# Performance work log

Measured on AMD Instinct MI355X. Metric: run time of the kernel, lower is better.

Reference implementation:

```python
import jax, jax.numpy as jnp
import numpy as np

N_NODES = 50000
N_EDGES = 800000
IN_FEATS = 128
H_FEATS = 128
NUM_CLASSES = 16


def setup_inputs() -> dict:
    key = jax.random.key(0)
    ks = jax.random.split(key, 10)
    in_feat = jax.random.normal(ks[0], (N_NODES, IN_FEATS), dtype=jnp.float32)
    src = jax.random.randint(ks[1], (N_EDGES,), 0, N_NODES, dtype=jnp.int64)
    dst = jax.random.randint(ks[2], (N_EDGES,), 0, N_NODES, dtype=jnp.int64)
    def glorot(k, shape):
        lim = np.sqrt(6.0 / (shape[0] + shape[1]))
        return jax.random.uniform(k, shape, jnp.float32, -lim, lim)
    W_self1 = glorot(ks[3], (IN_FEATS, H_FEATS))
    W_neigh1 = glorot(ks[4], (IN_FEATS, H_FEATS))
    b1 = jnp.zeros((H_FEATS,), jnp.float32)
    W_self2 = glorot(ks[5], (H_FEATS, NUM_CLASSES))
    W_neigh2 = glorot(ks[6], (H_FEATS, NUM_CLASSES))
    b2 = jnp.zeros((NUM_CLASSES,), jnp.float32)
    return {"in_feat": in_feat, "src": src, "dst": dst,
            "W_self1": W_self1, "W_neigh1": W_neigh1, "b1": b1,
            "W_self2": W_self2, "W_neigh2": W_neigh2, "b2": b2}


def _mean_agg(h, src, dst, n_nodes):
    # sum of source features at each destination node, divided by in-degree
    summed = jax.ops.segment_sum(h[src], dst, num_segments=n_nodes)  # [N, d]
    deg = jax.ops.segment_sum(jnp.ones_like(dst, dtype=h.dtype), dst,
                              num_segments=n_nodes)                   # [N]
    return summed / jnp.maximum(deg, 1.0)[:, None]


def _sage_conv(h, src, dst, W_self, W_neigh, b):
    h_neigh = _mean_agg(h, src, dst, h.shape[0])
    return h @ W_self + h_neigh @ W_neigh + b


def reference(in_feat, src, dst, W_self1, W_neigh1, b1, W_self2, W_neigh2, b2):
    h = _sage_conv(in_feat, src, dst, W_self1, W_neigh1, b1)
    h = jax.nn.relu(h)
    h = _sage_conv(h, src, dst, W_self2, W_neigh2, b2)
    return h
```

## Files before the change

kernel.cpp:

```cpp
#include <hip/hip_runtime.h>

#define NF 128
#define BSH 8
#define CHUNK 4096

typedef __attribute__((ext_vector_type(8))) short short8;
typedef __attribute__((ext_vector_type(4))) float floatx4;

__device__ __forceinline__ unsigned short f2bf(float f) {
    unsigned u = __float_as_uint(f);
    u += 0x7fff + ((u >> 16) & 1);
    return (unsigned short)(u >> 16);
}
__device__ __forceinline__ unsigned pk2(float a, float b) {
    return (unsigned)f2bf(a) | ((unsigned)f2bf(b) << 16);
}
__device__ __forceinline__ float bflo(unsigned u) { return __uint_as_float(u << 16); }
__device__ __forceinline__ float bfhi(unsigned u) { return __uint_as_float(u & 0xffff0000u); }

__device__ __forceinline__ unsigned enc8(float f) {
    unsigned b = __float_as_uint(f);
    unsigned s = (b >> 24) & 0x80u;
    b &= 0x7fffffffu;
    unsigned t = b + 0x7FFFFu + ((b >> 20) & 1u);
    unsigned m = (t >= 0x3C800000u) ? (((t - 0x3C000000u) >> 20) & 0x7Fu) : 0u;
    return s | m;
}
__device__ __forceinline__ void dec4(float* acc, unsigned w) {
#pragma unroll
    for (int j = 0; j < 4; ++j) {
        unsigned u = (w >> (8 * j)) & 0xffu;
        acc[j] += __uint_as_float(((u & 0x80u) << 24) | ((u & 0x7fu) << 20));
    }
}


__global__ __launch_bounds__(256) void k_prep(const float* __restrict__ in_feat,
                                              const int* __restrict__ dst,
                                              const float* __restrict__ Ws1,
                                              const float* __restrict__ Wn1,
                                              const float* __restrict__ Ws2,
                                              const float* __restrict__ Wn2,
                                              unsigned short* __restrict__ featbf,
                                              unsigned char* __restrict__ feat8,
                                              unsigned short* __restrict__ W1t,
                                              unsigned short* __restrict__ W2t,
                                              int* __restrict__ cnt2,
                                              int nb_cvt, int nb_w, int E) {
    int b = blockIdx.x, tid = threadIdx.x;
    if (b < nb_cvt) {
        int i = b * 256 + tid;
        const float4* p = (const float4*)in_feat + (size_t)i * 2;
        float4 a = p[0], c = p[1];
        uint4 o;
        o.x = pk2(a.x, a.y); o.y = pk2(a.z, a.w);
        o.z = pk2(c.x, c.y); o.w = pk2(c.z, c.w);
        ((uint4*)featbf)[i] = o;
        uint2 q;
        q.x = enc8(a.x) | (enc8(a.y) << 8) | (enc8(a.z) << 16) | (enc8(a.w) << 24);
        q.y = enc8(c.x) | (enc8(c.y) << 8) | (enc8(c.z) << 16) | (enc8(c.w) << 24);
        ((uint2*)feat8)[i] = q;
    } else if (b < nb_cvt + nb_w) {
        int idx = (b - nb_cvt) * 256 + tid;
        if (idx < 128 * 256) {
            int n = idx >> 8, kk = idx & 255;
            float v = (kk < 128) ? Ws1[(size_t)kk * 128 + n]
                                 : Wn1[(size_t)(kk - 128) * 128 + n];
            W1t[idx] = f2bf(v);
        } else {
            int idx2 = idx - 128 * 256;
            if (idx2 < 32 * 128) {
                int n = idx2 >> 7, k = idx2 & 127;
                float v = (n < 16) ? Ws2[(size_t)k * 16 + n]
                                   : Wn2[(size_t)k * 16 + (n - 16)];
                W2t[idx2] = f2bf(v);
            }
        }
    } else {
        __shared__ int h[256];
        int c = b - nb_cvt - nb_w;
        h[tid] = 0;
        __syncthreads();
        int base = c * CHUNK;
        int n = min(CHUNK, E - base);
        for (int i = tid; i < n; i += 256) atomicAdd(&h[dst[base + i] >> BSH], 1);
        __syncthreads();
        cnt2[c * 256 + tid] = h[tid];
    }
}


__global__ __launch_bounds__(256) void k_cscan(const int* __restrict__ cnt2,
                                               int* __restrict__ goff,
                                               int* __restrict__ basep, int nc) {
    __shared__ int sw[4];
    int tid = threadIdx.x, lane = tid & 63, w = tid >> 6;
    int tot = 0;
    int c = 0;
    for (; c + 7 < nc; c += 8) {
        int v0 = cnt2[(c + 0) * 256 + tid], v1 = cnt2[(c + 1) * 256 + tid];
        int v2 = cnt2[(c + 2) * 256 + tid], v3 = cnt2[(c + 3) * 256 + tid];
        int v4 = cnt2[(c + 4) * 256 + tid], v5 = cnt2[(c + 5) * 256 + tid];
        int v6 = cnt2[(c + 6) * 256 + tid], v7 = cnt2[(c + 7) * 256 + tid];
        tot += ((v0 + v1) + (v2 + v3)) + ((v4 + v5) + (v6 + v7));
    }
    for (; c < nc; ++c) tot += cnt2[c * 256 + tid];

    int inc = tot;
#pragma unroll
    for (int d = 1; d < 64; d <<= 1) {
        int t = __shfl_up(inc, (unsigned)d, 64);
        if (lane >= d) inc += t;
    }
    if (lane == 63) sw[w] = inc;
    __syncthreads();
    int add = 0;
    for (int i = 0; i < w; ++i) add += sw[i];
    int ex = add + inc - tot;
    goff[tid] = ex;
    if (tid == 255) goff[256] = ex + tot;

    int run = ex;
    for (c = 0; c < nc; c += 8) {
        int v[8];
#pragma unroll
        for (int j = 0; j < 8; ++j)
            v[j] = (c + j < nc) ? cnt2[(c + j) * 256 + tid] : 0;
#pragma unroll
        for (int j = 0; j < 8; ++j) {
            if (c + j < nc) basep[(c + j) * 256 + tid] = run;
            run += v[j];
        }
    }
}


__global__ __launch_bounds__(256) void k_part(const int* __restrict__ src,
                                              const int* __restrict__ dst,
                                              const int* __restrict__ basep,
                                              unsigned* __restrict__ ebuf, int E) {
    __shared__ int cur[256];
    int tid = threadIdx.x;
    cur[tid] = basep[blockIdx.x * 256 + tid];
    __syncthreads();
    int base = blockIdx.x * CHUNK;
    int n = min(CHUNK, E - base);
    for (int i = tid; i < n; i += 256) {
        int dd = dst[base + i];
        int p = atomicAdd(&cur[dd >> BSH], 1);
        ebuf[p] = ((unsigned)(dd & 255) << 16) | (unsigned)src[base + i];
    }
}


__global__ __launch_bounds__(256) void k_fine(const unsigned* __restrict__ ebuf,
                                              const int* __restrict__ goff,
                                              int* __restrict__ off,
                                              int* __restrict__ csr, int N) {
    __shared__ int degL[256];
    __shared__ int offL[256];
    __shared__ int sw[4];
    int b = blockIdx.x, tid = threadIdx.x;
    int node0 = b << BSH;
    int e0 = goff[b], e1 = goff[b + 1];
    degL[tid] = 0;
    __syncthreads();
    for (int e = e0 + tid; e < e1; e += 256) atomicAdd(&degL[ebuf[e] >> 16], 1);
    __syncthreads();
    int lane = tid & 63, w = tid >> 6;
    int v = degL[tid], inc = v;
#pragma unroll
    for (int d = 1; d < 64; d <<= 1) {
        int t = __shfl_up(inc, (unsigned)d, 64);
        if (lane >= d) inc += t;
    }
    if (lane == 63) sw[w] = inc;
    __syncthreads();
    int add = 0;
    for (int i = 0; i < w; ++i) add += sw[i];
    int ex = add + inc - v;
    offL[tid] = ex;
    int idx = node0 + tid;
    if (idx <= N) off[idx] = e0 + ex;
    degL[tid] = 0;
    __syncthreads();
    for (int e = e0 + tid; e < e1; e += 256) {
        unsigned u = ebuf[e];
        int d = u >> 16;
        int pos = e0 + offL[d] + atomicAdd(&degL[d], 1);
        csr[pos] = (int)(u & 0xffffu);
    }
}


__global__ __launch_bounds__(256, 6) void k_agg1(const unsigned char* __restrict__ feat8,
                                                 const int* __restrict__ off,
                                                 const int* __restrict__ csr,
                                                 unsigned short* __restrict__ outm, int N) {
    int idx = blockIdx.x * 256 + threadIdx.x;
    int g = idx >> 4;
    int lane = idx & 15;
    if (g >= N) return;
    int s0 = off[g], s1 = off[g + 1];
    float acc[8];
#pragma unroll
    for (int i = 0; i < 8; ++i) acc[i] = 0.f;
    const uint2* F = (const uint2*)feat8;
    int e = s0;
    for (; e + 7 < s1; e += 8) {
        uint2 v0 = F[(size_t)csr[e + 0] * 16 + lane];
        uint2 v1 = F[(size_t)csr[e + 1] * 16 + lane];
        uint2 v2 = F[(size_t)csr[e + 2] * 16 + lane];
        uint2 v3 = F[(size_t)csr[e + 3] * 16 + lane];
        uint2 v4 = F[(size_t)csr[e + 4] * 16 + lane];
        uint2 v5 = F[(size_t)csr[e + 5] * 16 + lane];
        uint2 v6 = F[(size_t)csr[e + 6] * 16 + lane];
        uint2 v7 = F[(size_t)csr[e + 7] * 16 + lane];
        dec4(acc + 0, v0.x); dec4(acc + 4, v0.y);
        dec4(acc + 0, v1.x); dec4(acc + 4, v1.y);
        dec4(acc + 0, v2.x); dec4(acc + 4, v2.y);
        dec4(acc + 0, v3.x); dec4(acc + 4, v3.y);
        dec4(acc + 0, v4.x); dec4(acc + 4, v4.y);
        dec4(acc + 0, v5.x); dec4(acc + 4, v5.y);
        dec4(acc + 0, v6.x); dec4(acc + 4, v6.y);
        dec4(acc + 0, v7.x); dec4(acc + 4, v7.y);
    }
    if (e + 3 < s1) {
        uint2 v0 = F[(size_t)csr[e + 0] * 16 + lane];
        uint2 v1 = F[(size_t)csr[e + 1] * 16 + lane];
        uint2 v2 = F[(size_t)csr[e + 2] * 16 + lane];
        uint2 v3 = F[(size_t)csr[e + 3] * 16 + lane];
        dec4(acc + 0, v0.x); dec4(acc + 4, v0.y);
        dec4(acc + 0, v1.x); dec4(acc + 4, v1.y);
        dec4(acc + 0, v2.x); dec4(acc + 4, v2.y);
        dec4(acc + 0, v3.x); dec4(acc + 4, v3.y);
        e += 4;
    }
    for (; e < s1; ++e) {
        uint2 v = F[(size_t)csr[e] * 16 + lane];
        dec4(acc + 0, v.x); dec4(acc + 4, v.y);
    }
    float inv = __uint_as_float(0x7B800000u) / fmaxf((float)(s1 - s0), 1.0f);
    uint2 o;
    o.x = pk2(acc[0] * inv, acc[1] * inv);
    o.y = pk2(acc[2] * inv, acc[3] * inv);
    uint2 o2;
    o2.x = pk2(acc[4] * inv, acc[5] * inv);
    o2.y = pk2(acc[6] * inv, acc[7] * inv);
    uint2* op = (uint2*)(outm + (size_t)g * NF + lane * 8);
    op[0] = o;
    op[1] = o2;
}


__global__ __launch_bounds__(256) void k_gemm(const unsigned short* __restrict__ Abf,
                                              const unsigned short* __restrict__ Hbf,
                                              const unsigned short* __restrict__ W1t,
                                              const float* __restrict__ b1,
                                              const unsigned short* __restrict__ W2t,
                                              const float* __restrict__ b2,
                                              float* __restrict__ t2s,
                                              unsigned short* __restrict__ t2n, int M) {
    __shared__ float hL[64 * 140];
    int tid = threadIdx.x;
    int w = tid >> 6, lane = tid & 63;
    int q = lane >> 4, r = lane & 15;
    int row = blockIdx.x * 64 + w * 16 + r;
    int rowc = min(row, M - 1);

    floatx4 acc[8];
#pragma unroll
    for (int t = 0; t < 8; ++t) acc[t] = (floatx4){0.f, 0.f, 0.f, 0.f};

    const unsigned short* arow = Abf + (size_t)rowc * 128;
    const unsigned short* hrow = Hbf + (size_t)rowc * 128;

#pragma unroll
    for (int kc = 0; kc < 8; ++kc) {
        const unsigned short* ap = (kc < 4) ? (arow + kc * 32 + q * 8)
                                            : (hrow + (kc - 4) * 32 + q * 8);
        short8 a = *(const short8*)ap;
        const unsigned short* wp = W1t + kc * 32 + q * 8 + (size_t)r * 256;
#pragma unroll
        for (int t = 0; t < 8; ++t) {
            short8 b = *(const short8*)(wp + (size_t)t * 16 * 256);
            acc[t] = __builtin_amdgcn_mfma_f32_16x16x32_bf16(a, b, acc[t], 0, 0, 0);
        }
    }

#pragma unroll
    for (int i = 0; i < 4; ++i) {
        int lr = w * 16 + q * 4 + i;
#pragma unroll
        for (int t = 0; t < 8; ++t)
            hL[lr * 140 + t * 16 + r] = fmaxf(acc[t][i] + b1[t * 16 + r], 0.0f);
    }

    floatx4 acc2[2];
#pragma unroll
    for (int t = 0; t < 2; ++t) acc2[t] = (floatx4){0.f, 0.f, 0.f, 0.f};

#pragma unroll
    for (int kc = 0; kc < 4; ++kc) {
        const float* pa = hL + (w * 16 + r) * 140 + kc * 32 + q * 8;
        float4 fa = *(const float4*)pa;
        float4 fb = *(const float4*)(pa + 4);
        union { short8 s; uint4 u; } cv;
        cv.u = make_uint4(pk2(fa.x, fa.y), pk2(fa.z, fa.w),
                          pk2(fb.x, fb.y), pk2(fb.z, fb.w));
        const unsigned short* wp = W2t + kc * 32 + q * 8 + (size_t)r * 128;
#pragma unroll
        for (int t = 0; t < 2; ++t) {
            short8 b = *(const short8*)(wp + (size_t)t * 16 * 128);
            acc2[t] = __builtin_amdgcn_mfma_f32_16x16x32_bf16(cv.s, b, acc2[t], 0, 0, 0);
        }
    }

    int orow0 = blockIdx.x * 64 + w * 16 + q * 4;
    float bb = b2[r];
#pragma unroll
    for (int i = 0; i < 4; ++i) {
        int orow = orow0 + i;
        if (orow < M) {
            t2s[(size_t)orow * 16 + r] = acc2[0][i] + bb;
            t2n[(size_t)orow * 16 + r] = f2bf(acc2[1][i]);
        }
    }
}


__global__ __launch_bounds__(256, 6) void k_out(const float* __restrict__ t2s,
                                                const unsigned short* __restrict__ t2n,
                                                const int* __restrict__ off,
                                                const int* __restrict__ csr,
                                                float* __restrict__ out, int N) {
    int idx = blockIdx.x * 256 + threadIdx.x;
    int node = idx >> 2;
    if (node >= N) return;
    int ln = idx & 3;
    int s0 = off[node], s1 = off[node + 1];
    float acc[4];
#pragma unroll
    for (int i = 0; i < 4; ++i) acc[i] = 0.f;
    const uint2* T = (const uint2*)t2n;
    int e = s0;
    for (; e + 7 < s1; e += 8) {
        uint2 v0 = T[(size_t)csr[e + 0] * 4 + ln];
        uint2 v1 = T[(size_t)csr[e + 1] * 4 + ln];
        uint2 v2 = T[(size_t)csr[e + 2] * 4 + ln];
        uint2 v3 = T[(size_t)csr[e + 3] * 4 + ln];
        uint2 v4 = T[(size_t)csr[e + 4] * 4 + ln];
        uint2 v5 = T[(size_t)csr[e + 5] * 4 + ln];
        uint2 v6 = T[(size_t)csr[e + 6] * 4 + ln];
        uint2 v7 = T[(size_t)csr[e + 7] * 4 + ln];
        acc[0] += bflo(v0.x) + bflo(v1.x) + bflo(v2.x) + bflo(v3.x)
                + bflo(v4.x) + bflo(v5.x) + bflo(v6.x) + bflo(v7.x);
        acc[1] += bfhi(v0.x) + bfhi(v1.x) + bfhi(v2.x) + bfhi(v3.x)
                + bfhi(v4.x) + bfhi(v5.x) + bfhi(v6.x) + bfhi(v7.x);
        acc[2] += bflo(v0.y) + bflo(v1.y) + bflo(v2.y) + bflo(v3.y)
                + bflo(v4.y) + bflo(v5.y) + bflo(v6.y) + bflo(v7.y);
        acc[3] += bfhi(v0.y) + bfhi(v1.y) + bfhi(v2.y) + bfhi(v3.y)
                + bfhi(v4.y) + bfhi(v5.y) + bfhi(v6.y) + bfhi(v7.y);
    }
    for (; e < s1; ++e) {
        uint2 v = T[(size_t)csr[e] * 4 + ln];
        acc[0] += bflo(v.x); acc[1] += bfhi(v.x);
        acc[2] += bflo(v.y); acc[3] += bfhi(v.y);
    }
    float inv = 1.0f / fmaxf((float)(s1 - s0), 1.0f);
    const float4* sp = (const float4*)(t2s + (size_t)node * 16 + ln * 4);
    float4 sv = sp[0];
    float4 r;
    r.x = sv.x + acc[0] * inv;
    r.y = sv.y + acc[1] * inv;
    r.z = sv.z + acc[2] * inv;
    r.w = sv.w + acc[3] * inv;
    *(float4*)(out + (size_t)node * 16 + ln * 4) = r;
}


extern "C" void kernel_launch(void* const* d_in, const int* in_sizes, int n_in,
                              void* d_out, int out_size, void* d_ws, size_t ws_size,
                              hipStream_t stream) {
    const float* in_feat = (const float*)d_in[0];
    const int*   src     = (const int*)d_in[1];
    const int*   dst     = (const int*)d_in[2];
    const float* Ws1     = (const float*)d_in[3];
    const float* Wn1     = (const float*)d_in[4];
    const float* b1      = (const float*)d_in[5];
    const float* Ws2     = (const float*)d_in[6];
    const float* Wn2     = (const float*)d_in[7];
    const float* b2      = (const float*)d_in[8];
    float* outp = (float*)d_out;

    int N = in_sizes[0] / NF;
    int E = in_sizes[1];
    int nb = (N + 255) >> BSH;
    int nc = (E + CHUNK - 1) / CHUNK;

    char* ws = (char*)d_ws;
    size_t o = 0;
    auto alloc = [&](size_t bytes) -> char* {
        char* p = ws + o;
        o = (o + bytes + 255) & ~(size_t)255;
        return p;
    };
    int*      cnt2  = (int*)alloc((size_t)nc * 256 * 4);
    int*      basep = (int*)alloc((size_t)nc * 256 * 4);
    int*      goff  = (int*)alloc(257 * 4);
    int*      off   = (int*)alloc((size_t)(N + 1) * 4);
    int*      csr   = (int*)alloc((size_t)E * 4);
    unsigned* ebuf  = (unsigned*)alloc((size_t)E * 4);
    unsigned short* featbf = (unsigned short*)alloc((size_t)N * NF * 2);
    unsigned char*  feat8  = (unsigned char*)alloc((size_t)N * NF);
    unsigned short* hn1    = (unsigned short*)alloc((size_t)N * NF * 2);
    unsigned short* W1t    = (unsigned short*)alloc((size_t)128 * 256 * 2);
    unsigned short* W2t    = (unsigned short*)alloc((size_t)32 * 128 * 2);
    float*          t2s    = (float*)alloc((size_t)N * 16 * 4);
    unsigned short* t2n    = (unsigned short*)alloc((size_t)N * 16 * 2);

    int nb_cvt = (N * NF / 8 + 255) / 256;
    int nb_w = (128 * 256 + 32 * 128 + 255) / 256;
    k_prep<<<nb_cvt + nb_w + nc, 256, 0, stream>>>(in_feat, dst, Ws1, Wn1, Ws2, Wn2,
                                                   featbf, feat8, W1t, W2t, cnt2,
                                                   nb_cvt, nb_w, E);
    k_cscan<<<1, 256, 0, stream>>>(cnt2, goff, basep, nc);
    k_part<<<nc, 256, 0, stream>>>(src, dst, basep, ebuf, E);
    k_fine<<<nb, 256, 0, stream>>>(ebuf, goff, off, csr, N);

    k_agg1<<<(N * 16 + 255) / 256, 256, 0, stream>>>(feat8, off, csr, hn1, N);

    int gb_m = (N + 63) / 64;
    k_gemm<<<gb_m, 256, 0, stream>>>(featbf, hn1, W1t, b1, W2t, b2, t2s, t2n, N);
    k_out<<<(N * 4 + 255) / 256, 256, 0, stream>>>(t2s, t2n, off, csr, outp, N);
}
```

Baseline: 218.6 us.

## Split layer-1 aggregation into two feature-half passes for cache locality

The first aggregation kernel now launches two sets of blocks, one per 64-byte half of each node's fp8 feature row, with 8 lanes per node instead of 16. Each pass only gathers half of each 128-byte row, which roughly halves the gathered working set per pass and is meant to improve L2 hit rates on the random neighbor gathers. Outputs become single 16-byte stores. The trade-off is that the CSR offsets and indices are read twice. The output kernel's launch-bounds occupancy hint is also raised from 6 to 8.

```diff
diff --git a/kernel.cpp b/kernel.cpp
--- a/kernel.cpp
+++ b/kernel.cpp
@@ -196,26 +196,29 @@
 __global__ __launch_bounds__(256, 6) void k_agg1(const unsigned char* __restrict__ feat8,
                                                  const int* __restrict__ off,
                                                  const int* __restrict__ csr,
-                                                 unsigned short* __restrict__ outm, int N) {
-    int idx = blockIdx.x * 256 + threadIdx.x;
-    int g = idx >> 4;
-    int lane = idx & 15;
+                                                 unsigned short* __restrict__ hn1,
+                                                 int N, int pb) {
+    int b = blockIdx.x;
+    int half = (b >= pb) ? 1 : 0;
+    int idx = (b - half * pb) * 256 + threadIdx.x;
+    int g = idx >> 3;
+    int lane = idx & 7;
     if (g >= N) return;
     int s0 = off[g], s1 = off[g + 1];
+    const unsigned char* base = feat8 + half * 64 + lane * 8;
     float acc[8];
 #pragma unroll
     for (int i = 0; i < 8; ++i) acc[i] = 0.f;
-    const uint2* F = (const uint2*)feat8;
     int e = s0;
     for (; e + 7 < s1; e += 8) {
-        uint2 v0 = F[(size_t)csr[e + 0] * 16 + lane];
-        uint2 v1 = F[(size_t)csr[e + 1] * 16 + lane];
-        uint2 v2 = F[(size_t)csr[e + 2] * 16 + lane];
-        uint2 v3 = F[(size_t)csr[e + 3] * 16 + lane];
-        uint2 v4 = F[(size_t)csr[e + 4] * 16 + lane];
-        uint2 v5 = F[(size_t)csr[e + 5] * 16 + lane];
-        uint2 v6 = F[(size_t)csr[e + 6] * 16 + lane];
-        uint2 v7 = F[(size_t)csr[e + 7] * 16 + lane];
+        uint2 v0 = *(const uint2*)(base + (size_t)csr[e + 0] * 128);
+        uint2 v1 = *(const uint2*)(base + (size_t)csr[e + 1] * 128);
+        uint2 v2 = *(const uint2*)(base + (size_t)csr[e + 2] * 128);
+        uint2 v3 = *(const uint2*)(base + (size_t)csr[e + 3] * 128);
+        uint2 v4 = *(const uint2*)(base + (size_t)csr[e + 4] * 128);
+        uint2 v5 = *(const uint2*)(base + (size_t)csr[e + 5] * 128);
+        uint2 v6 = *(const uint2*)(base + (size_t)csr[e + 6] * 128);
+        uint2 v7 = *(const uint2*)(base + (size_t)csr[e + 7] * 128);
         dec4(acc + 0, v0.x); dec4(acc + 4, v0.y);
         dec4(acc + 0, v1.x); dec4(acc + 4, v1.y);
         dec4(acc + 0, v2.x); dec4(acc + 4, v2.y);
@@ -226,10 +229,10 @@
         dec4(acc + 0, v7.x); dec4(acc + 4, v7.y);
     }
     if (e + 3 < s1) {
-        uint2 v0 = F[(size_t)csr[e + 0] * 16 + lane];
-        uint2 v1 = F[(size_t)csr[e + 1] * 16 + lane];
-        uint2 v2 = F[(size_t)csr[e + 2] * 16 + lane];
-        uint2 v3 = F[(size_t)csr[e + 3] * 16 + lane];
+        uint2 v0 = *(const uint2*)(base + (size_t)csr[e + 0] * 128);
+        uint2 v1 = *(const uint2*)(base + (size_t)csr[e + 1] * 128);
+        uint2 v2 = *(const uint2*)(base + (size_t)csr[e + 2] * 128);
+        uint2 v3 = *(const uint2*)(base + (size_t)csr[e + 3] * 128);
         dec4(acc + 0, v0.x); dec4(acc + 4, v0.y);
         dec4(acc + 0, v1.x); dec4(acc + 4, v1.y);
         dec4(acc + 0, v2.x); dec4(acc + 4, v2.y);
@@ -237,19 +240,16 @@
         e += 4;
     }
     for (; e < s1; ++e) {
-        uint2 v = F[(size_t)csr[e] * 16 + lane];
+        uint2 v = *(const uint2*)(base + (size_t)csr[e] * 128);
         dec4(acc + 0, v.x); dec4(acc + 4, v.y);
     }
     float inv = __uint_as_float(0x7B800000u) / fmaxf((float)(s1 - s0), 1.0f);
-    uint2 o;
+    uint4 o;
     o.x = pk2(acc[0] * inv, acc[1] * inv);
     o.y = pk2(acc[2] * inv, acc[3] * inv);
-    uint2 o2;
-    o2.x = pk2(acc[4] * inv, acc[5] * inv);
-    o2.y = pk2(acc[6] * inv, acc[7] * inv);
-    uint2* op = (uint2*)(outm + (size_t)g * NF + lane * 8);
-    op[0] = o;
-    op[1] = o2;
+    o.z = pk2(acc[4] * inv, acc[5] * inv);
+    o.w = pk2(acc[6] * inv, acc[7] * inv);
+    *(uint4*)(hn1 + (size_t)g * NF + half * 64 + lane * 8) = o;
 }
 
 
@@ -329,7 +329,7 @@
 }
 
 
-__global__ __launch_bounds__(256, 6) void k_out(const float* __restrict__ t2s,
+__global__ __launch_bounds__(256, 8) void k_out(const float* __restrict__ t2s,
                                                 const unsigned short* __restrict__ t2n,
                                                 const int* __restrict__ off,
                                                 const int* __restrict__ csr,
@@ -428,7 +428,8 @@
     k_part<<<nc, 256, 0, stream>>>(src, dst, basep, ebuf, E);
     k_fine<<<nb, 256, 0, stream>>>(ebuf, goff, off, csr, N);
 
-    k_agg1<<<(N * 16 + 255) / 256, 256, 0, stream>>>(feat8, off, csr, hn1, N);
+    int pb = (N * 8 + 255) / 256;
+    k_agg1<<<pb * 2, 256, 0, stream>>>(feat8, off, csr, hn1, N, pb);
 
     int gb_m = (N + 63) / 64;
     k_gemm<<<gb_m, 256, 0, stream>>>(featbf, hn1, W1t, b1, W2t, b2, t2s, t2n, N);
```

After: 222.0 us. No clear change (+1.6%).
